# Kernel tuning notes

Measured on AMD Instinct MI355X. Metric: run time of the kernel, lower is better.

Reference implementation:

```python
import jax, jax.numpy as jnp
import numpy as np

EPS = 1e-5
DN = ('NCHW', 'OIHW', 'NCHW')


def _conv(x, w):
    return jax.lax.conv_general_dilated(x, w, (1, 1), 'SAME', dimension_numbers=DN)


def _bn(x, g, b, m, v):
    # eval-mode batchnorm over channel axis 1
    inv = jax.lax.rsqrt(v + EPS)
    return (x - m[:, None, None]) * (g * inv)[:, None, None] + b[:, None, None]


def setup_inputs() -> dict:
    key = jax.random.key(0)
    ks = jax.random.split(key, 32)
    dim, mid, B, H, W = 256, 128, 4, 128, 128
    d = {}
    d['x'] = jax.random.normal(ks[0], (B, dim, H, W), dtype=jnp.float32)

    def bn_params(i, c):
        return (jax.random.uniform(ks[i], (c,), dtype=jnp.float32) + 0.5,
                jax.random.normal(ks[i + 1], (c,), dtype=jnp.float32) * 0.1,
                jax.random.normal(ks[i + 2], (c,), dtype=jnp.float32) * 0.1,
                jax.random.uniform(ks[i + 3], (c,), dtype=jnp.float32) + 0.5)

    d['w_p1'] = jax.random.normal(ks[1], (mid, dim, 3, 3), dtype=jnp.float32) * 0.02
    d['g_p1'], d['b_p1'], d['m_p1'], d['v_p1'] = bn_params(2, mid)
    d['w_p2'] = jax.random.normal(ks[6], (mid, dim, 3, 3), dtype=jnp.float32) * 0.02
    d['g_p2'], d['b_p2'], d['m_p2'], d['v_p2'] = bn_params(7, mid)
    d['w_c1'] = jax.random.normal(ks[11], (dim, mid, 3, 3), dtype=jnp.float32) * 0.02
    d['g_c1'], d['b_c1'], d['m_c1'], d['v_c1'] = bn_params(12, dim)
    d['w_c2'] = jax.random.normal(ks[16], (dim, dim, 1, 1), dtype=jnp.float32) * 0.02
    d['g_c2'], d['b_c2'], d['m_c2'], d['v_c2'] = bn_params(17, dim)
    d['w_p3'] = jax.random.normal(ks[21], (dim, dim, 3, 3), dtype=jnp.float32) * 0.02
    d['g_p3'], d['b_p3'], d['m_p3'], d['v_p3'] = bn_params(22, dim)
    return d


def reference(x,
              w_p1, g_p1, b_p1, m_p1, v_p1,
              w_p2, g_p2, b_p2, m_p2, v_p2,
              w_c1, g_c1, b_c1, m_c1, v_c1,
              w_c2, g_c2, b_c2, m_c2, v_c2,
              w_p3, g_p3, b_p3, m_p3, v_p3):
    # conv-bn-relu branches (dim -> 128)
    p1 = jax.nn.relu(_bn(_conv(x, w_p1), g_p1, b_p1, m_p1, v_p1))
    p2 = jax.nn.relu(_bn(_conv(x, w_p2), g_p2, b_p2, m_p2, v_p2))
    # corner pooling: 'top' = reverse cummax over H (axis 2),
    #                 'left' = reverse cummax over W (axis 3)
    cp1 = jax.lax.cummax(p1, axis=2, reverse=True)
    cp2 = jax.lax.cummax(p2, axis=3, reverse=True)
    bn1 = _bn(_conv(cp1 + cp2, w_c1), g_c1, b_c1, m_c1, v_c1)
    bn2 = _bn(_conv(x, w_c2), g_c2, b_c2, m_c2, v_c2)
    r = jax.nn.relu(bn1 + bn2)
    out = jax.nn.relu(_bn(_conv(r, w_p3), g_p3, b_p3, m_p3, v_p3))
    return out
```

## Files before the change

### kernel.cpp

```cpp
#include <hip/hip_runtime.h>
#include <math.h>

#define HH 128
#define WW 128
#define HWSZ (128*128)

typedef __attribute__((ext_vector_type(8))) short short8;
typedef __attribute__((ext_vector_type(4))) float float4v;

__device__ inline short f2bf(float f) {
  unsigned x = __float_as_uint(f);
  unsigned r = (x + 0x7fffu + ((x >> 16) & 1u)) >> 16;
  return (short)r;
}
__device__ inline float bf2f(unsigned short u) {
  return __uint_as_float(((unsigned)u) << 16);
}
__device__ inline int swz(int row, int g) {
  return row * 32 + ((g ^ ((row >> 1) & 3)) << 3);
}

__global__ __launch_bounds__(256) void xcvt_kernel(const float* __restrict__ x,
                                                   short* __restrict__ xbf) {
  __shared__ short tile[32 * 264];
  const int t = threadIdx.x;
  const int h = blockIdx.x, b = blockIdx.y;
  for (int wc = 0; wc < 4; wc++) {
    const int w0 = wc * 32;
    __syncthreads();
    #pragma unroll
    for (int coi = 0; coi < 8; coi++) {
      int ci = coi * 32 + (t >> 3);
      int wq = t & 7;
      float4v f = *(const float4v*)&x[((size_t)b * 256 + ci) * HWSZ + h * WW + w0 + wq * 4];
      tile[(wq * 4 + 0) * 264 + ci] = f2bf(f.x);
      tile[(wq * 4 + 1) * 264 + ci] = f2bf(f.y);
      tile[(wq * 4 + 2) * 264 + ci] = f2bf(f.z);
      tile[(wq * 4 + 3) * 264 + ci] = f2bf(f.w);
    }
    __syncthreads();
    #pragma unroll
    for (int pass = 0; pass < 4; pass++) {
      int wl = pass * 8 + (t >> 5);
      int ci8 = (t & 31) * 8;
      short8 v = *(const short8*)&tile[wl * 264 + ci8];
      *(short8*)&xbf[(((size_t)b * HH + h) * WW + w0 + wl) * 256 + ci8] = v;
    }
  }
}

__global__ void wcvt3_kernel(const float* __restrict__ w, const float* __restrict__ g,
                             const float* __restrict__ v, short* __restrict__ out,
                             int Cin, int CoutW, int co_off) {
  int idx = blockIdx.x * blockDim.x + threadIdx.x;
  int total = CoutW * Cin * 9;
  if (idx >= total) return;
  int t  = idx % 9;
  int ci = (idx / 9) % Cin;
  int co = idx / (9 * Cin);
  float s = g[co] * rsqrtf(v[co] + 1e-5f);
  out[((size_t)t * 256 + co_off + co) * Cin + ci] = f2bf(w[idx] * s);
}

__global__ void wcvt1_kernel(const float* __restrict__ w, const float* __restrict__ g,
                             const float* __restrict__ v, short* __restrict__ out,
                             int Cin, int CoutW) {
  int idx = blockIdx.x * blockDim.x + threadIdx.x;
  if (idx >= CoutW * Cin) return;
  int co = idx / Cin;
  float s = g[co] * rsqrtf(v[co] + 1e-5f);
  out[idx] = f2bf(w[idx] * s);
}

template<int CIN_A, bool PHASE_B, int SHIFT_MODE, bool SPLIT_OUT, bool OUT_F32>
__global__ __launch_bounds__(256, 2) void conv_mfma(
    const short* __restrict__ srcA, const short* __restrict__ xB,
    const short* __restrict__ wbA, const short* __restrict__ wbB,
    const float* __restrict__ g0, const float* __restrict__ b0,
    const float* __restrict__ m0, const float* __restrict__ v0,
    const float* __restrict__ g1, const float* __restrict__ b1,
    const float* __restrict__ m1, const float* __restrict__ v1,
    void* __restrict__ out0, void* __restrict__ out1)
{
  __shared__ short A_s[130 * 32];
  __shared__ short B_s[3 * 256 * 32];

  const int tid  = threadIdx.x;
  const int wave = tid >> 6;
  const int lane = tid & 63;
  const int wm = wave & 1;
  const int wn = wave >> 1;
  const int lr = lane & 15;
  const int lk = lane >> 4;

  const int h  = blockIdx.x & 127;
  const int b  = blockIdx.x >> 7;

  constexpr int ncA = CIN_A / 32;
  const int dystart = (h == 0) ? 1 : 0;
  const int dyend   = (h == HH - 1) ? 2 : 3;
  const int chunksA = (dyend - dystart) * ncA;
  const int total   = chunksA + (PHASE_B ? 8 : 0);

  float4v acc[4][8];
  #pragma unroll
  for (int i = 0; i < 4; i++)
    #pragma unroll
    for (int j = 0; j < 8; j++) acc[i][j] = (float4v)(0.0f);

  short8 rA[3], rB[12];
  const short* aRow = nullptr;
  const short* bBase = nullptr;
  bool curIsA = true;

  auto decode = [&](int t, const short*& ar, const short*& bb, bool& isA) {
    isA = (t < chunksA);
    if (isA) {
      int dy  = dystart + t / ncA;
      int ci0 = (t % ncA) * 32;
      ar = srcA + (((size_t)b * HH + (h + dy - 1)) * WW) * CIN_A + ci0;
      bb = wbA + ((size_t)(dy * 3) * 256) * CIN_A + ci0;
    } else {
      int ci0 = (t - chunksA) * 32;
      ar = xB + (((size_t)b * HH + h) * WW) * 256 + ci0;
      bb = wbB + ci0;
    }
  };

  auto loadRegs = [&](const short* ar, const short* bb, bool isA) {
    if (isA) {
      #pragma unroll
      for (int i = 0; i < 2; i++) {
        int idx = tid + i * 256;
        int w = (idx >> 2) - 1, q = idx & 3;
        rA[i] = ((unsigned)w < (unsigned)WW)
                  ? *(const short8*)(ar + (size_t)w * CIN_A + q * 8) : (short8)(0);
      }
      if (tid < 8) {
        int idx = tid + 512;
        int w = (idx >> 2) - 1, q = idx & 3;
        rA[2] = ((unsigned)w < (unsigned)WW)
                  ? *(const short8*)(ar + (size_t)w * CIN_A + q * 8) : (short8)(0);
      }
      #pragma unroll
      for (int i = 0; i < 12; i++) {
        int idx = tid + i * 256;
        int dx = idx >> 10, rem = idx & 1023;
        int co = rem >> 2, q = rem & 3;
        rB[i] = *(const short8*)(bb + (size_t)(dx * 256 + co) * CIN_A + q * 8);
      }
    } else {
      #pragma unroll
      for (int i = 0; i < 2; i++) {
        int idx = tid + i * 256;
        int wp = idx >> 2, q = idx & 3;
        rA[i] = *(const short8*)(ar + (size_t)wp * 256 + q * 8);
      }
      #pragma unroll
      for (int i = 0; i < 4; i++) {
        int idx = tid + i * 256;
        int co = idx >> 2, q = idx & 3;
        rB[i] = *(const short8*)(bb + (size_t)co * 256 + q * 8);
      }
    }
  };

  auto storeLDS = [&](bool isA) {
    if (isA) {
      #pragma unroll
      for (int i = 0; i < 2; i++) {
        int idx = tid + i * 256;
        *(short8*)&A_s[swz(idx >> 2, idx & 3)] = rA[i];
      }
      if (tid < 8) {
        int idx = tid + 512;
        *(short8*)&A_s[swz(idx >> 2, idx & 3)] = rA[2];
      }
      #pragma unroll
      for (int i = 0; i < 12; i++) {
        int idx = tid + i * 256;
        int dx = idx >> 10, rem = idx & 1023;
        *(short8*)&B_s[swz(dx * 256 + (rem >> 2), rem & 3)] = rB[i];
      }
    } else {
      #pragma unroll
      for (int i = 0; i < 2; i++) {
        int idx = tid + i * 256;
        *(short8*)&A_s[swz(idx >> 2, idx & 3)] = rA[i];
      }
      #pragma unroll
      for (int i = 0; i < 4; i++) {
        int idx = tid + i * 256;
        *(short8*)&B_s[swz(idx >> 2, idx & 3)] = rB[i];
      }
    }
  };

  decode(0, aRow, bBase, curIsA);
  loadRegs(aRow, bBase, curIsA);

  for (int t = 0; t < total; t++) {
    bool isA = curIsA;
    __syncthreads();
    storeLDS(isA);
    __syncthreads();
    if (t + 1 < total) {
      decode(t + 1, aRow, bBase, curIsA);
      loadRegs(aRow, bBase, curIsA);
    }
    const int ndx = isA ? 3 : 1;
    for (int dx = 0; dx < ndx; dx++) {
      short8 af[4];
      #pragma unroll
      for (int mi = 0; mi < 4; mi++)
        af[mi] = *(const short8*)&A_s[swz(wm * 64 + mi * 16 + lr + dx, lk)];
      #pragma unroll
      for (int ni = 0; ni < 8; ni++) {
        short8 bfr = *(const short8*)&B_s[swz(dx * 256 + wn * 128 + ni * 16 + lr, lk)];
        #pragma unroll
        for (int mi = 0; mi < 4; mi++)
          acc[mi][ni] = __builtin_amdgcn_mfma_f32_16x16x32_bf16(af[mi], bfr, acc[mi][ni], 0, 0, 0);
      }
    }
  }

  #pragma unroll
  for (int ni = 0; ni < 8; ni++) {
    int c = wn * 128 + ni * 16 + lr;
    float sh;
    if (SHIFT_MODE == 0) {
      float s = g0[c] * rsqrtf(v0[c] + 1e-5f);
      sh = b0[c] - m0[c] * s;
    } else if (SHIFT_MODE == 1) {
      int cc = c & 127;
      const float* gg = (c < 128) ? g0 : g1;
      const float* bb = (c < 128) ? b0 : b1;
      const float* mm = (c < 128) ? m0 : m1;
      const float* vv = (c < 128) ? v0 : v1;
      float s = gg[cc] * rsqrtf(vv[cc] + 1e-5f);
      sh = bb[cc] - mm[cc] * s;
    } else {
      float s0 = g0[c] * rsqrtf(v0[c] + 1e-5f);
      float s1 = g1[c] * rsqrtf(v1[c] + 1e-5f);
      sh = (b0[c] - m0[c] * s0) + (b1[c] - m1[c] * s1);
    }
    #pragma unroll
    for (int mi = 0; mi < 4; mi++) {
      int px = wm * 64 + mi * 16 + lk * 4;
      float4v v = acc[mi][ni];
      v.x = fmaxf(v.x + sh, 0.0f);
      v.y = fmaxf(v.y + sh, 0.0f);
      v.z = fmaxf(v.z + sh, 0.0f);
      v.w = fmaxf(v.w + sh, 0.0f);
      if (OUT_F32) {
        float* ob = (float*)out0;
        *(float4v*)(ob + ((size_t)b * 256 + c) * HWSZ + (size_t)h * WW + px) = v;
      } else if (SPLIT_OUT) {
        short* ob = (short*)((c < 128) ? out0 : out1);
        size_t base = (((size_t)b * HH + h) * WW + px) * 128 + (c & 127);
        ob[base      ] = f2bf(v.x);
        ob[base + 128 ] = f2bf(v.y);
        ob[base + 256 ] = f2bf(v.z);
        ob[base + 384 ] = f2bf(v.w);
      } else {
        short* ob = (short*)out0;
        size_t base = (((size_t)b * HH + h) * WW + px) * 256 + c;
        ob[base      ] = f2bf(v.x);
        ob[base + 256 ] = f2bf(v.y);
        ob[base + 512 ] = f2bf(v.z);
        ob[base + 768 ] = f2bf(v.w);
      }
    }
  }
}

__global__ void colscan_kernel(unsigned* __restrict__ p) {
  const int t = threadIdx.x;
  const int wl = t >> 6, cp = t & 63;
  const int w = blockIdx.x * 4 + wl;
  const int b = blockIdx.y;
  float m0 = -INFINITY, m1 = -INFINITY;
  for (int h = HH - 1; h >= 0; h--) {
    size_t idx = (((size_t)b * HH + h) * WW + w) * 64 + cp;
    unsigned u = p[idx];
    float f0 = bf2f((unsigned short)(u & 0xffff));
    float f1 = bf2f((unsigned short)(u >> 16));
    m0 = fmaxf(m0, f0);
    m1 = fmaxf(m1, f1);
    p[idx] = ((unsigned)(unsigned short)f2bf(m1) << 16) | (unsigned short)f2bf(m0);
  }
}

__global__ __launch_bounds__(256) void rowscan_add_kernel(
    const short* __restrict__ p2, short* __restrict__ p1) {
  __shared__ short pl[128 * 128];
  const int tid = threadIdx.x;
  const int hb = blockIdx.x;
  const int b  = blockIdx.y;
  const size_t base = (((size_t)b * HH + hb) * WW) * 128;

  #pragma unroll
  for (int i = 0; i < 8; i++) {
    int idx = tid + i * 256;
    *(short8*)&pl[idx * 8] = *(const short8*)(p2 + base + (size_t)idx * 8);
  }
  __syncthreads();
  if (tid < 128) {
    float m = -INFINITY;
    for (int w = WW - 1; w >= 0; w--) {
      int a = w * 128 + tid;
      m = fmaxf(m, bf2f((unsigned short)pl[a]));
      pl[a] = (short)f2bf(m);
    }
  }
  __syncthreads();
  #pragma unroll
  for (int i = 0; i < 8; i++) {
    int idx = tid + i * 256;
    short8 sv = *(const short8*)&pl[idx * 8];
    short8 ov = *(const short8*)(p1 + base + (size_t)idx * 8);
    short8 rv;
    #pragma unroll
    for (int j = 0; j < 8; j++)
      rv[j] = f2bf(bf2f((unsigned short)sv[j]) + bf2f((unsigned short)ov[j]));
    *(short8*)(p1 + base + (size_t)idx * 8) = rv;
  }
}

extern "C" void kernel_launch(void* const* d_in, const int* in_sizes, int n_in,
                              void* d_out, int out_size, void* d_ws, size_t ws_size,
                              hipStream_t stream) {
  const float* x    = (const float*)d_in[0];
  const float* w_p1 = (const float*)d_in[1];
  const float* g_p1 = (const float*)d_in[2];
  const float* b_p1 = (const float*)d_in[3];
  const float* m_p1 = (const float*)d_in[4];
  const float* v_p1 = (const float*)d_in[5];
  const float* w_p2 = (const float*)d_in[6];
  const float* g_p2 = (const float*)d_in[7];
  const float* b_p2 = (const float*)d_in[8];
  const float* m_p2 = (const float*)d_in[9];
  const float* v_p2 = (const float*)d_in[10];
  const float* w_c1 = (const float*)d_in[11];
  const float* g_c1 = (const float*)d_in[12];
  const float* b_c1 = (const float*)d_in[13];
  const float* m_c1 = (const float*)d_in[14];
  const float* v_c1 = (const float*)d_in[15];
  const float* w_c2 = (const float*)d_in[16];
  const float* g_c2 = (const float*)d_in[17];
  const float* b_c2 = (const float*)d_in[18];
  const float* m_c2 = (const float*)d_in[19];
  const float* v_c2 = (const float*)d_in[20];
  const float* w_p3 = (const float*)d_in[21];
  const float* g_p3 = (const float*)d_in[22];
  const float* b_p3 = (const float*)d_in[23];
  const float* m_p3 = (const float*)d_in[24];
  const float* v_p3 = (const float*)d_in[25];

  char* ws = (char*)d_ws;
  short* p1  = (short*)(ws + 0);
  short* p2  = (short*)(ws + 16777216);
  short* r   = (short*)(ws + 33554432);
  short* xbf = (short*)(ws + 67108864);
  short* wb12 = r;
  short* wbc1 = p2;
  short* wbc2 = (short*)(ws + 16777216 + 589824);
  short* wbp3 = p1;

  xcvt_kernel<<<dim3(128, 4), 256, 0, stream>>>(x, xbf);

  wcvt3_kernel<<<(128 * 256 * 9 + 255) / 256, 256, 0, stream>>>(w_p1, g_p1, v_p1, wb12, 256, 128, 0);
  wcvt3_kernel<<<(128 * 256 * 9 + 255) / 256, 256, 0, stream>>>(w_p2, g_p2, v_p2, wb12, 256, 128, 128);

  conv_mfma<256, false, 1, true, false><<<dim3(512), 256, 0, stream>>>(
      xbf, nullptr, wb12, nullptr,
      g_p1, b_p1, m_p1, v_p1, g_p2, b_p2, m_p2, v_p2, (void*)p1, (void*)p2);

  colscan_kernel<<<dim3(32, 4), 256, 0, stream>>>((unsigned*)p1);
  rowscan_add_kernel<<<dim3(128, 4), 256, 0, stream>>>(p2, p1);

  wcvt3_kernel<<<(256 * 128 * 9 + 255) / 256, 256, 0, stream>>>(w_c1, g_c1, v_c1, wbc1, 128, 256, 0);
  wcvt1_kernel<<<(256 * 256 + 255) / 256, 256, 0, stream>>>(w_c2, g_c2, v_c2, wbc2, 256, 256);

  conv_mfma<128, true, 2, false, false><<<dim3(512), 256, 0, stream>>>(
      p1, xbf, wbc1, wbc2,
      g_c1, b_c1, m_c1, v_c1, g_c2, b_c2, m_c2, v_c2, (void*)r, nullptr);

  wcvt3_kernel<<<(256 * 256 * 9 + 255) / 256, 256, 0, stream>>>(w_p3, g_p3, v_p3, wbp3, 256, 256, 0);

  conv_mfma<256, false, 0, false, true><<<dim3(512), 256, 0, stream>>>(
      r, nullptr, wbp3, nullptr,
      g_p3, b_p3, m_p3, v_p3, nullptr, nullptr, nullptr, nullptr, d_out, nullptr);
}
```

Baseline: 425.7 us.

## Double-buffer LDS, process two output rows per 512-thread block in conv

The conv kernel now uses 512 threads per block, with each block computing two output rows so each weight chunk loaded into LDS is reused across both rows. LDS is double-buffered: the next chunk's global loads are issued before the MFMAs, and the stores to LDS are interleaved between the dx sub-steps under s_setprio. This cuts the loop to one barrier per chunk. Block IDs are remapped to spread work across XCDs, and the grid is halved to 256 blocks. The cost is doubled LDS (about 114 KB per block) and fewer blocks, which may limit occupancy and leave a 256-CU device with only one wave of blocks.

```diff
diff --git a/kernel.cpp b/kernel.cpp
--- a/kernel.cpp
+++ b/kernel.cpp
@@ -73,17 +73,17 @@
 }
 
 template<int CIN_A, bool PHASE_B, int SHIFT_MODE, bool SPLIT_OUT, bool OUT_F32>
-__global__ __launch_bounds__(256, 2) void conv_mfma(
+__global__ __launch_bounds__(512, 2) void conv_mfma(
     const short* __restrict__ srcA, const short* __restrict__ xB,
     const short* __restrict__ wbA, const short* __restrict__ wbB,
     const float* __restrict__ g0, const float* __restrict__ b0,
-    const float* __restrict__ m0, const float* __restrict__ v0,
+    const float* __restrict__ m0, const float* __restrict__ v0p,
     const float* __restrict__ g1, const float* __restrict__ b1,
-    const float* __restrict__ m1, const float* __restrict__ v1,
+    const float* __restrict__ m1, const float* __restrict__ v1p,
     void* __restrict__ out0, void* __restrict__ out1)
 {
-  __shared__ short A_s[130 * 32];
-  __shared__ short B_s[3 * 256 * 32];
+  __shared__ short A_s[2 * 8320];
+  __shared__ short B_s[2 * 24576];
 
   const int tid  = threadIdx.x;
   const int wave = tid >> 6;
@@ -93,160 +93,201 @@
   const int lr = lane & 15;
   const int lk = lane >> 4;
 
-  const int h  = blockIdx.x & 127;
-  const int b  = blockIdx.x >> 7;
+  const int raw = blockIdx.x;
+  const int id  = (raw & 7) * 32 + (raw >> 3);
+  const int h0  = (id & 63) * 2;
+  const int b   = id >> 6;
 
   constexpr int ncA = CIN_A / 32;
-  const int dystart = (h == 0) ? 1 : 0;
-  const int dyend   = (h == HH - 1) ? 2 : 3;
-  const int chunksA = (dyend - dystart) * ncA;
-  const int total   = chunksA + (PHASE_B ? 8 : 0);
-
-  float4v acc[4][8];
+  constexpr int chunksA = 3 * ncA;
+  constexpr int total = chunksA + (PHASE_B ? 8 : 0);
+
+  float4v acc[8][4];
   #pragma unroll
-  for (int i = 0; i < 4; i++)
-    #pragma unroll
-    for (int j = 0; j < 8; j++) acc[i][j] = (float4v)(0.0f);
-
-  short8 rA[3], rB[12];
-  const short* aRow = nullptr;
-  const short* bBase = nullptr;
-  bool curIsA = true;
-
-  auto decode = [&](int t, const short*& ar, const short*& bb, bool& isA) {
-    isA = (t < chunksA);
-    if (isA) {
-      int dy  = dystart + t / ncA;
-      int ci0 = (t % ncA) * 32;
-      ar = srcA + (((size_t)b * HH + (h + dy - 1)) * WW) * CIN_A + ci0;
-      bb = wbA + ((size_t)(dy * 3) * 256) * CIN_A + ci0;
+  for (int i = 0; i < 8; i++)
+    #pragma unroll
+    for (int j = 0; j < 4; j++) acc[i][j] = (float4v)(0.0f);
+
+  short8 rA[3], rB[6];
+  bool nIsA = true, av0 = false, av1 = false;
+  const short* aR = nullptr;
+  const short* bB = nullptr;
+  int r0 = 0;
+
+  auto decode = [&](int t) {
+    nIsA = (t < chunksA);
+    if (nIsA) {
+      int dy = t / ncA, ci0 = (t % ncA) * 32;
+      r0  = h0 + dy - 1;
+      av0 = (r0 >= 0);
+      av1 = (r0 + 1 <= HH - 1);
+      aR = srcA + ((size_t)b * HH) * WW * CIN_A + ci0;
+      bB = wbA + (size_t)(dy * 3) * 256 * CIN_A + ci0;
     } else {
       int ci0 = (t - chunksA) * 32;
-      ar = xB + (((size_t)b * HH + h) * WW) * 256 + ci0;
-      bb = wbB + ci0;
-    }
-  };
-
-  auto loadRegs = [&](const short* ar, const short* bb, bool isA) {
+      aR = xB + (((size_t)b * HH + h0) * WW) * 256 + ci0;
+      bB = wbB + ci0;
+    }
+  };
+
+  auto issueLoads = [&]() {
+    if (nIsA) {
+      int rr0 = av0 ? r0 : 0;
+      int rr1 = av1 ? r0 + 1 : 0;
+      { int g = tid; int w = (g >> 2) - 1, q = g & 3;
+        rA[0] = (av0 && (unsigned)w < (unsigned)WW)
+            ? *(const short8*)(aR + ((size_t)rr0 * WW + w) * CIN_A + q * 8) : (short8)(0); }
+      { int g = tid + 512; int pl = (g >= 520) ? 1 : 0; int gg = g - pl * 520;
+        int w = (gg >> 2) - 1, q = gg & 3;
+        bool vv = pl ? av1 : av0; int rr = pl ? rr1 : rr0;
+        rA[1] = (vv && (unsigned)w < (unsigned)WW)
+            ? *(const short8*)(aR + ((size_t)rr * WW + w) * CIN_A + q * 8) : (short8)(0); }
+      if (tid < 16) { int gg = tid + 504; int w = (gg >> 2) - 1, q = gg & 3;
+        rA[2] = (av1 && (unsigned)w < (unsigned)WW)
+            ? *(const short8*)(aR + ((size_t)rr1 * WW + w) * CIN_A + q * 8) : (short8)(0); }
+      #pragma unroll
+      for (int i = 0; i < 6; i++) {
+        int idx = tid + i * 512;
+        int dx = idx >> 10, rem = idx & 1023, co = rem >> 2, q = rem & 3;
+        rB[i] = *(const short8*)(bB + (size_t)(dx * 256 + co) * CIN_A + q * 8);
+      }
+    } else {
+      #pragma unroll
+      for (int i = 0; i < 2; i++) {
+        int idx = tid + i * 512; int pl = idx >> 9, rem = idx & 511, w = rem >> 2, q = rem & 3;
+        rA[i] = *(const short8*)(aR + ((size_t)pl * WW + w) * 256 + q * 8);
+      }
+      #pragma unroll
+      for (int i = 0; i < 2; i++) {
+        int idx = tid + i * 512; int co = idx >> 2, q = idx & 3;
+        rB[i] = *(const short8*)(bB + (size_t)co * 256 + q * 8);
+      }
+    }
+  };
+
+  int cur = 1;
+
+  auto storeP0 = [&]() {
+    short* Ab = A_s + (cur ^ 1) * 8320;
+    short* Bb = B_s + (cur ^ 1) * 24576;
+    if (nIsA) {
+      { int g = tid; *(short8*)&Ab[swz(g >> 2, g & 3)] = rA[0]; }
+      { int g = tid + 512; int pl = (g >= 520) ? 1 : 0; int gg = g - pl * 520;
+        *(short8*)&Ab[pl * 4160 + swz(gg >> 2, gg & 3)] = rA[1]; }
+      if (tid < 16) { int gg = tid + 504;
+        *(short8*)&Ab[4160 + swz(gg >> 2, gg & 3)] = rA[2]; }
+      #pragma unroll
+      for (int i = 0; i < 2; i++) {
+        int idx = tid + i * 512; int dx = idx >> 10, rem = idx & 1023;
+        *(short8*)&Bb[swz(dx * 256 + (rem >> 2), rem & 3)] = rB[i];
+      }
+    } else {
+      #pragma unroll
+      for (int i = 0; i < 2; i++) {
+        int idx = tid + i * 512; int pl = idx >> 9, rem = idx & 511;
+        *(short8*)&Ab[pl * 4160 + swz(rem >> 2, rem & 3)] = rA[i];
+      }
+      #pragma unroll
+      for (int i = 0; i < 2; i++) {
+        int idx = tid + i * 512;
+        *(short8*)&Bb[swz(idx >> 2, idx & 3)] = rB[i];
+      }
+    }
+  };
+  auto storeP1 = [&]() {
+    if (!nIsA) return;
+    short* Bb = B_s + (cur ^ 1) * 24576;
+    #pragma unroll
+    for (int i = 2; i < 4; i++) {
+      int idx = tid + i * 512; int dx = idx >> 10, rem = idx & 1023;
+      *(short8*)&Bb[swz(dx * 256 + (rem >> 2), rem & 3)] = rB[i];
+    }
+  };
+  auto storeP2 = [&]() {
+    if (!nIsA) return;
+    short* Bb = B_s + (cur ^ 1) * 24576;
+    #pragma unroll
+    for (int i = 4; i < 6; i++) {
+      int idx = tid + i * 512; int dx = idx >> 10, rem = idx & 1023;
+      *(short8*)&Bb[swz(dx * 256 + (rem >> 2), rem & 3)] = rB[i];
+    }
+  };
+
+  auto mfma_dx = [&](int dx) {
+    const short* Ab = A_s + cur * 8320 + wm * 4160;
+    const short* Bb = B_s + cur * 24576;
+    short8 bfv[4];
+    #pragma unroll
+    for (int ni = 0; ni < 4; ni++)
+      bfv[ni] = *(const short8*)&Bb[swz(dx * 256 + wn * 64 + ni * 16 + lr, lk)];
+    #pragma unroll
+    for (int mi = 0; mi < 8; mi++) {
+      short8 afv = *(const short8*)&Ab[swz(mi * 16 + lr + dx, lk)];
+      #pragma unroll
+      for (int ni = 0; ni < 4; ni++)
+        acc[mi][ni] = __builtin_amdgcn_mfma_f32_16x16x32_bf16(afv, bfv[ni], acc[mi][ni], 0, 0, 0);
+    }
+  };
+
+  decode(0);
+  issueLoads();
+  storeP0(); storeP1(); storeP2();
+  asm volatile("s_waitcnt lgkmcnt(0)" ::: "memory");
+  __builtin_amdgcn_s_barrier();
+  __builtin_amdgcn_sched_barrier(0);
+  cur = 0;
+
+  #pragma unroll 1
+  for (int t = 0; t < total; t++) {
+    const bool isA = (t < chunksA);
+    const bool hnext = (t + 1 < total);
+    if (hnext) { decode(t + 1); issueLoads(); }
+
+    __builtin_amdgcn_s_setprio(1);
+    mfma_dx(0);
+    __builtin_amdgcn_s_setprio(0);
+    if (hnext) storeP0();
     if (isA) {
-      #pragma unroll
-      for (int i = 0; i < 2; i++) {
-        int idx = tid + i * 256;
-        int w = (idx >> 2) - 1, q = idx & 3;
-        rA[i] = ((unsigned)w < (unsigned)WW)
-                  ? *(const short8*)(ar + (size_t)w * CIN_A + q * 8) : (short8)(0);
-      }
-      if (tid < 8) {
-        int idx = tid + 512;
-        int w = (idx >> 2) - 1, q = idx & 3;
-        rA[2] = ((unsigned)w < (unsigned)WW)
-                  ? *(const short8*)(ar + (size_t)w * CIN_A + q * 8) : (short8)(0);
-      }
-      #pragma unroll
-      for (int i = 0; i < 12; i++) {
-        int idx = tid + i * 256;
-        int dx = idx >> 10, rem = idx & 1023;
-        int co = rem >> 2, q = rem & 3;
-        rB[i] = *(const short8*)(bb + (size_t)(dx * 256 + co) * CIN_A + q * 8);
-      }
-    } else {
-      #pragma unroll
-      for (int i = 0; i < 2; i++) {
-        int idx = tid + i * 256;
-        int wp = idx >> 2, q = idx & 3;
-        rA[i] = *(const short8*)(ar + (size_t)wp * 256 + q * 8);
-      }
-      #pragma unroll
-      for (int i = 0; i < 4; i++) {
-        int idx = tid + i * 256;
-        int co = idx >> 2, q = idx & 3;
-        rB[i] = *(const short8*)(bb + (size_t)co * 256 + q * 8);
-      }
-    }
-  };
-
-  auto storeLDS = [&](bool isA) {
-    if (isA) {
-      #pragma unroll
-      for (int i = 0; i < 2; i++) {
-        int idx = tid + i * 256;
-        *(short8*)&A_s[swz(idx >> 2, idx & 3)] = rA[i];
-      }
-      if (tid < 8) {
-        int idx = tid + 512;
-        *(short8*)&A_s[swz(idx >> 2, idx & 3)] = rA[2];
-      }
-      #pragma unroll
-      for (int i = 0; i < 12; i++) {
-        int idx = tid + i * 256;
-        int dx = idx >> 10, rem = idx & 1023;
-        *(short8*)&B_s[swz(dx * 256 + (rem >> 2), rem & 3)] = rB[i];
-      }
-    } else {
-      #pragma unroll
-      for (int i = 0; i < 2; i++) {
-        int idx = tid + i * 256;
-        *(short8*)&A_s[swz(idx >> 2, idx & 3)] = rA[i];
-      }
-      #pragma unroll
-      for (int i = 0; i < 4; i++) {
-        int idx = tid + i * 256;
-        *(short8*)&B_s[swz(idx >> 2, idx & 3)] = rB[i];
-      }
-    }
-  };
-
-  decode(0, aRow, bBase, curIsA);
-  loadRegs(aRow, bBase, curIsA);
-
-  for (int t = 0; t < total; t++) {
-    bool isA = curIsA;
-    __syncthreads();
-    storeLDS(isA);
-    __syncthreads();
-    if (t + 1 < total) {
-      decode(t + 1, aRow, bBase, curIsA);
-      loadRegs(aRow, bBase, curIsA);
-    }
-    const int ndx = isA ? 3 : 1;
-    for (int dx = 0; dx < ndx; dx++) {
-      short8 af[4];
-      #pragma unroll
-      for (int mi = 0; mi < 4; mi++)
-        af[mi] = *(const short8*)&A_s[swz(wm * 64 + mi * 16 + lr + dx, lk)];
-      #pragma unroll
-      for (int ni = 0; ni < 8; ni++) {
-        short8 bfr = *(const short8*)&B_s[swz(dx * 256 + wn * 128 + ni * 16 + lr, lk)];
-        #pragma unroll
-        for (int mi = 0; mi < 4; mi++)
-          acc[mi][ni] = __builtin_amdgcn_mfma_f32_16x16x32_bf16(af[mi], bfr, acc[mi][ni], 0, 0, 0);
-      }
-    }
-  }
-
+      __builtin_amdgcn_s_setprio(1);
+      mfma_dx(1);
+      __builtin_amdgcn_s_setprio(0);
+      if (hnext) storeP1();
+      __builtin_amdgcn_s_setprio(1);
+      mfma_dx(2);
+      __builtin_amdgcn_s_setprio(0);
+      if (hnext) storeP2();
+    } else if (hnext) { storeP1(); storeP2(); }
+
+    asm volatile("s_waitcnt lgkmcnt(0)" ::: "memory");
+    __builtin_amdgcn_s_barrier();
+    __builtin_amdgcn_sched_barrier(0);
+    cur ^= 1;
+  }
+
+  const int h2 = h0 + wm;
   #pragma unroll
-  for (int ni = 0; ni < 8; ni++) {
-    int c = wn * 128 + ni * 16 + lr;
+  for (int ni = 0; ni < 4; ni++) {
+    int c = wn * 64 + ni * 16 + lr;
     float sh;
     if (SHIFT_MODE == 0) {
-      float s = g0[c] * rsqrtf(v0[c] + 1e-5f);
+      float s = g0[c] * rsqrtf(v0p[c] + 1e-5f);
       sh = b0[c] - m0[c] * s;
     } else if (SHIFT_MODE == 1) {
       int cc = c & 127;
       const float* gg = (c < 128) ? g0 : g1;
       const float* bb = (c < 128) ? b0 : b1;
       const float* mm = (c < 128) ? m0 : m1;
-      const float* vv = (c < 128) ? v0 : v1;
+      const float* vv = (c < 128) ? v0p : v1p;
       float s = gg[cc] * rsqrtf(vv[cc] + 1e-5f);
       sh = bb[cc] - mm[cc] * s;
     } else {
-      float s0 = g0[c] * rsqrtf(v0[c] + 1e-5f);
-      float s1 = g1[c] * rsqrtf(v1[c] + 1e-5f);
+      float s0 = g0[c] * rsqrtf(v0p[c] + 1e-5f);
+      float s1 = g1[c] * rsqrtf(v1p[c] + 1e-5f);
       sh = (b0[c] - m0[c] * s0) + (b1[c] - m1[c] * s1);
     }
     #pragma unroll
-    for (int mi = 0; mi < 4; mi++) {
-      int px = wm * 64 + mi * 16 + lk * 4;
+    for (int mi = 0; mi < 8; mi++) {
+      int w = mi * 16 + lk * 4;
       float4v v = acc[mi][ni];
       v.x = fmaxf(v.x + sh, 0.0f);
       v.y = fmaxf(v.y + sh, 0.0f);
@@ -254,17 +295,17 @@
       v.w = fmaxf(v.w + sh, 0.0f);
       if (OUT_F32) {
         float* ob = (float*)out0;
-        *(float4v*)(ob + ((size_t)b * 256 + c) * HWSZ + (size_t)h * WW + px) = v;
+        *(float4v*)(ob + ((size_t)b * 256 + c) * HWSZ + (size_t)h2 * WW + w) = v;
       } else if (SPLIT_OUT) {
         short* ob = (short*)((c < 128) ? out0 : out1);
-        size_t base = (((size_t)b * HH + h) * WW + px) * 128 + (c & 127);
+        size_t base = (((size_t)b * HH + h2) * WW + w) * 128 + (c & 127);
         ob[base      ] = f2bf(v.x);
         ob[base + 128 ] = f2bf(v.y);
         ob[base + 256 ] = f2bf(v.z);
         ob[base + 384 ] = f2bf(v.w);
       } else {
         short* ob = (short*)out0;
-        size_t base = (((size_t)b * HH + h) * WW + px) * 256 + c;
+        size_t base = (((size_t)b * HH + h2) * WW + w) * 256 + c;
         ob[base      ] = f2bf(v.x);
         ob[base + 256 ] = f2bf(v.y);
         ob[base + 512 ] = f2bf(v.z);
@@ -372,7 +413,7 @@
   wcvt3_kernel<<<(128 * 256 * 9 + 255) / 256, 256, 0, stream>>>(w_p1, g_p1, v_p1, wb12, 256, 128, 0);
   wcvt3_kernel<<<(128 * 256 * 9 + 255) / 256, 256, 0, stream>>>(w_p2, g_p2, v_p2, wb12, 256, 128, 128);
 
-  conv_mfma<256, false, 1, true, false><<<dim3(512), 256, 0, stream>>>(
+  conv_mfma<256, false, 1, true, false><<<dim3(256), 512, 0, stream>>>(
       xbf, nullptr, wb12, nullptr,
       g_p1, b_p1, m_p1, v_p1, g_p2, b_p2, m_p2, v_p2, (void*)p1, (void*)p2);
 
@@ -382,13 +423,13 @@
   wcvt3_kernel<<<(256 * 128 * 9 + 255) / 256, 256, 0, stream>>>(w_c1, g_c1, v_c1, wbc1, 128, 256, 0);
   wcvt1_kernel<<<(256 * 256 + 255) / 256, 256, 0, stream>>>(w_c2, g_c2, v_c2, wbc2, 256, 256);
 
-  conv_mfma<128, true, 2, false, false><<<dim3(512), 256, 0, stream>>>(
+  conv_mfma<128, true, 2, false, false><<<dim3(256), 512, 0, stream>>>(
       p1, xbf, wbc1, wbc2,
       g_c1, b_c1, m_c1, v_c1, g_c2, b_c2, m_c2, v_c2, (void*)r, nullptr);
 
   wcvt3_kernel<<<(256 * 256 * 9 + 255) / 256, 256, 0, stream>>>(w_p3, g_p3, v_p3, wbp3, 256, 256, 0);
 
-  conv_mfma<256, false, 0, false, true><<<dim3(512), 256, 0, stream>>>(
+  conv_mfma<256, false, 0, false, true><<<dim3(256), 512, 0, stream>>>(
       r, nullptr, wbp3, nullptr,
       g_p3, b_p3, m_p3, v_p3, nullptr, nullptr, nullptr, nullptr, d_out, nullptr);
 }
```

After: 722.2 us. +69.7%, slower.

## Double-buffer LDS and interleave prefetch with MFMA in conv mainloop

Applied to the files above, without the earlier changes.

Converts the conv mainloop from a single LDS buffer with two barriers per chunk to a double-buffered LDS scheme. The next chunk's register data is stored into the alternate buffer between the per-dx MFMA groups, while global loads for the chunk after that are issued, leaving one barrier per iteration. Splitting the weight load and store into two halves spreads the memory traffic across the compute phases. This doubles LDS use to about 112 KB per block, so launch bounds drop to one block per SM and occupancy falls.

```diff
diff --git a/kernel.cpp b/kernel.cpp
--- a/kernel.cpp
+++ b/kernel.cpp
@@ -73,7 +73,7 @@
 }
 
 template<int CIN_A, bool PHASE_B, int SHIFT_MODE, bool SPLIT_OUT, bool OUT_F32>
-__global__ __launch_bounds__(256, 2) void conv_mfma(
+__global__ __launch_bounds__(256, 1) void conv_mfma(
     const short* __restrict__ srcA, const short* __restrict__ xB,
     const short* __restrict__ wbA, const short* __restrict__ wbB,
     const float* __restrict__ g0, const float* __restrict__ b0,
@@ -82,8 +82,8 @@
     const float* __restrict__ m1, const float* __restrict__ v1,
     void* __restrict__ out0, void* __restrict__ out1)
 {
-  __shared__ short A_s[130 * 32];
-  __shared__ short B_s[3 * 256 * 32];
+  __shared__ short A_s[2][130 * 32];
+  __shared__ short B_s[2][3 * 256 * 32];
 
   const int tid  = threadIdx.x;
   const int wave = tid >> 6;
@@ -109,12 +109,9 @@
     for (int j = 0; j < 8; j++) acc[i][j] = (float4v)(0.0f);
 
   short8 rA[3], rB[12];
-  const short* aRow = nullptr;
-  const short* bBase = nullptr;
-  bool curIsA = true;
-
-  auto decode = [&](int t, const short*& ar, const short*& bb, bool& isA) {
-    isA = (t < chunksA);
+
+  auto decode = [&](int t, const short*& ar, const short*& bb) -> bool {
+    bool isA = (t < chunksA);
     if (isA) {
       int dy  = dystart + t / ncA;
       int ci0 = (t % ncA) * 32;
@@ -125,9 +122,10 @@
       ar = xB + (((size_t)b * HH + h) * WW) * 256 + ci0;
       bb = wbB + ci0;
     }
-  };
-
-  auto loadRegs = [&](const short* ar, const short* bb, bool isA) {
+    return isA;
+  };
+
+  auto loadA = [&](const short* ar, bool isA) {
     if (isA) {
       #pragma unroll
       for (int i = 0; i < 2; i++) {
@@ -142,8 +140,20 @@
         rA[2] = ((unsigned)w < (unsigned)WW)
                   ? *(const short8*)(ar + (size_t)w * CIN_A + q * 8) : (short8)(0);
       }
-      #pragma unroll
-      for (int i = 0; i < 12; i++) {
+    } else {
+      #pragma unroll
+      for (int i = 0; i < 2; i++) {
+        int idx = tid + i * 256;
+        int wp = idx >> 2, q = idx & 3;
+        rA[i] = *(const short8*)(ar + (size_t)wp * 256 + q * 8);
+      }
+    }
+  };
+
+  auto loadB1 = [&](const short* bb, bool isA) {
+    if (isA) {
+      #pragma unroll
+      for (int i = 0; i < 6; i++) {
         int idx = tid + i * 256;
         int dx = idx >> 10, rem = idx & 1023;
         int co = rem >> 2, q = rem & 3;
@@ -151,12 +161,6 @@
       }
     } else {
       #pragma unroll
-      for (int i = 0; i < 2; i++) {
-        int idx = tid + i * 256;
-        int wp = idx >> 2, q = idx & 3;
-        rA[i] = *(const short8*)(ar + (size_t)wp * 256 + q * 8);
-      }
-      #pragma unroll
       for (int i = 0; i < 4; i++) {
         int idx = tid + i * 256;
         int co = idx >> 2, q = idx & 3;
@@ -165,63 +169,125 @@
     }
   };
 
-  auto storeLDS = [&](bool isA) {
+  auto loadB2 = [&](const short* bb, bool isA) {
+    if (isA) {
+      #pragma unroll
+      for (int i = 6; i < 12; i++) {
+        int idx = tid + i * 256;
+        int dx = idx >> 10, rem = idx & 1023;
+        int co = rem >> 2, q = rem & 3;
+        rB[i] = *(const short8*)(bb + (size_t)(dx * 256 + co) * CIN_A + q * 8);
+      }
+    }
+  };
+
+  auto storeA = [&](int buf, bool isA) {
+    short* As = A_s[buf];
     if (isA) {
       #pragma unroll
       for (int i = 0; i < 2; i++) {
         int idx = tid + i * 256;
-        *(short8*)&A_s[swz(idx >> 2, idx & 3)] = rA[i];
+        *(short8*)&As[swz(idx >> 2, idx & 3)] = rA[i];
       }
       if (tid < 8) {
         int idx = tid + 512;
-        *(short8*)&A_s[swz(idx >> 2, idx & 3)] = rA[2];
-      }
-      #pragma unroll
-      for (int i = 0; i < 12; i++) {
+        *(short8*)&As[swz(idx >> 2, idx & 3)] = rA[2];
+      }
+    } else {
+      #pragma unroll
+      for (int i = 0; i < 2; i++) {
+        int idx = tid + i * 256;
+        *(short8*)&As[swz(idx >> 2, idx & 3)] = rA[i];
+      }
+    }
+  };
+
+  auto storeB1 = [&](int buf, bool isA) {
+    short* Bs = B_s[buf];
+    if (isA) {
+      #pragma unroll
+      for (int i = 0; i < 6; i++) {
         int idx = tid + i * 256;
         int dx = idx >> 10, rem = idx & 1023;
-        *(short8*)&B_s[swz(dx * 256 + (rem >> 2), rem & 3)] = rB[i];
-      }
-    } else {
-      #pragma unroll
-      for (int i = 0; i < 2; i++) {
-        int idx = tid + i * 256;
-        *(short8*)&A_s[swz(idx >> 2, idx & 3)] = rA[i];
-      }
+        *(short8*)&Bs[swz(dx * 256 + (rem >> 2), rem & 3)] = rB[i];
+      }
+    } else {
       #pragma unroll
       for (int i = 0; i < 4; i++) {
         int idx = tid + i * 256;
-        *(short8*)&B_s[swz(idx >> 2, idx & 3)] = rB[i];
-      }
-    }
-  };
-
-  decode(0, aRow, bBase, curIsA);
-  loadRegs(aRow, bBase, curIsA);
-
+        *(short8*)&Bs[swz(idx >> 2, idx & 3)] = rB[i];
+      }
+    }
+  };
+
+  auto storeB2 = [&](int buf, bool isA) {
+    short* Bs = B_s[buf];
+    if (isA) {
+      #pragma unroll
+      for (int i = 6; i < 12; i++) {
+        int idx = tid + i * 256;
+        int dx = idx >> 10, rem = idx & 1023;
+        *(short8*)&Bs[swz(dx * 256 + (rem >> 2), rem & 3)] = rB[i];
+      }
+    }
+  };
+
+  auto mfma_dx = [&](int buf, int dx) {
+    short8 af[4];
+    #pragma unroll
+    for (int mi = 0; mi < 4; mi++)
+      af[mi] = *(const short8*)&A_s[buf][swz(wm * 64 + mi * 16 + lr + dx, lk)];
+    #pragma unroll
+    for (int ni = 0; ni < 8; ni++) {
+      short8 bfr = *(const short8*)&B_s[buf][swz(dx * 256 + wn * 128 + ni * 16 + lr, lk)];
+      #pragma unroll
+      for (int mi = 0; mi < 4; mi++)
+        acc[mi][ni] = __builtin_amdgcn_mfma_f32_16x16x32_bf16(af[mi], bfr, acc[mi][ni], 0, 0, 0);
+    }
+  };
+
+  {
+    const short* ar; const short* bb;
+    bool ia0 = decode(0, ar, bb);
+    loadA(ar, ia0); loadB1(bb, ia0); loadB2(bb, ia0);
+    storeA(0, ia0); storeB1(0, ia0); storeB2(0, ia0);
+    if (total > 1) {
+      const short* ar1; const short* bb1;
+      bool ia1 = decode(1, ar1, bb1);
+      loadA(ar1, ia1); loadB1(bb1, ia1); loadB2(bb1, ia1);
+    }
+    asm volatile("s_waitcnt lgkmcnt(0)" ::: "memory");
+    __builtin_amdgcn_s_barrier();
+    __builtin_amdgcn_sched_barrier(0);
+  }
+
+  int cur = 0;
+  #pragma unroll 1
   for (int t = 0; t < total; t++) {
-    bool isA = curIsA;
-    __syncthreads();
-    storeLDS(isA);
-    __syncthreads();
-    if (t + 1 < total) {
-      decode(t + 1, aRow, bBase, curIsA);
-      loadRegs(aRow, bBase, curIsA);
-    }
-    const int ndx = isA ? 3 : 1;
-    for (int dx = 0; dx < ndx; dx++) {
-      short8 af[4];
-      #pragma unroll
-      for (int mi = 0; mi < 4; mi++)
-        af[mi] = *(const short8*)&A_s[swz(wm * 64 + mi * 16 + lr + dx, lk)];
-      #pragma unroll
-      for (int ni = 0; ni < 8; ni++) {
-        short8 bfr = *(const short8*)&B_s[swz(dx * 256 + wn * 128 + ni * 16 + lr, lk)];
-        #pragma unroll
-        for (int mi = 0; mi < 4; mi++)
-          acc[mi][ni] = __builtin_amdgcn_mfma_f32_16x16x32_bf16(af[mi], bfr, acc[mi][ni], 0, 0, 0);
-      }
-    }
+    const bool isA = (t < chunksA);
+    const bool h1  = (t + 1 < total);
+    const bool sA  = (t + 1 < chunksA);
+    const bool h2  = (t + 2 < total);
+
+    const short* ar2 = nullptr; const short* bb2 = nullptr; bool ia2 = false;
+    if (h2) ia2 = decode(t + 2, ar2, bb2);
+
+    mfma_dx(cur, 0);
+    if (h1) storeA(cur ^ 1, sA);
+    if (h2) loadA(ar2, ia2);
+
+    if (isA) mfma_dx(cur, 1);
+    if (h1) storeB1(cur ^ 1, sA);
+    if (h2) loadB1(bb2, ia2);
+
+    if (isA) mfma_dx(cur, 2);
+    if (h1) storeB2(cur ^ 1, sA);
+    if (h2) loadB2(bb2, ia2);
+
+    asm volatile("s_waitcnt lgkmcnt(0)" ::: "memory");
+    __builtin_amdgcn_s_barrier();
+    __builtin_amdgcn_sched_barrier(0);
+    cur ^= 1;
   }
 
   #pragma unroll
```

Result: slower. 520.9 us (+22.4%).

## Parallelize corner-pool scans with wavefront shuffle prefix-max in LDS

Applied to the files above, without the earlier changes.

Both the column (top) and row (left) reverse cummax kernels now stage a 128x128 slice into padded float LDS and run a wavefront-wide suffix-max scan using shuffles over two 64-element halves. Previously the column scan ran 128 sequential strided global loads per thread with only 128 blocks, and the row scan used only 128 of 256 threads doing a serial 128-step loop. The change targets these latency-bound serial scans. In exchange it adds 66 KB of LDS per block, which limits occupancy, and adds extra shuffle work.

```diff
diff --git a/kernel.cpp b/kernel.cpp
--- a/kernel.cpp
+++ b/kernel.cpp
@@ -274,26 +274,57 @@
   }
 }
 
-__global__ void colscan_kernel(unsigned* __restrict__ p) {
-  const int t = threadIdx.x;
-  const int wl = t >> 6, cp = t & 63;
-  const int w = blockIdx.x * 4 + wl;
+__global__ __launch_bounds__(256) void colscan_kernel(short* __restrict__ p) {
+  __shared__ float xf[128 * 129];
+  const int tid = threadIdx.x;
+  const int w = blockIdx.x;
   const int b = blockIdx.y;
-  float m0 = -INFINITY, m1 = -INFINITY;
-  for (int h = HH - 1; h >= 0; h--) {
-    size_t idx = (((size_t)b * HH + h) * WW + w) * 64 + cp;
-    unsigned u = p[idx];
-    float f0 = bf2f((unsigned short)(u & 0xffff));
-    float f1 = bf2f((unsigned short)(u >> 16));
-    m0 = fmaxf(m0, f0);
-    m1 = fmaxf(m1, f1);
-    p[idx] = ((unsigned)(unsigned short)f2bf(m1) << 16) | (unsigned short)f2bf(m0);
+  const size_t base = (size_t)b * HH * WW * 128 + (size_t)w * 128;
+
+  #pragma unroll
+  for (int i = 0; i < 8; i++) {
+    int idx = tid + i * 256;
+    int h = idx >> 4, g = idx & 15;
+    short8 v = *(const short8*)(p + base + (size_t)h * (WW * 128) + g * 8);
+    #pragma unroll
+    for (int j = 0; j < 8; j++) xf[h * 129 + g * 8 + j] = bf2f((unsigned short)v[j]);
+  }
+  __syncthreads();
+
+  const int lane = tid & 63, wv = tid >> 6;
+  for (int rep = 0; rep < 32; rep++) {
+    int c = rep * 4 + wv;
+    float lo = xf[lane * 129 + c];
+    float hi = xf[(lane + 64) * 129 + c];
+    #pragma unroll
+    for (int off = 1; off < 64; off <<= 1) {
+      int src = lane + off; if (src > 63) src = 63;
+      float ul = __shfl(lo, src);
+      float uh = __shfl(hi, src);
+      lo = fmaxf(lo, ul);
+      hi = fmaxf(hi, uh);
+    }
+    float ht = __shfl(hi, 0);
+    lo = fmaxf(lo, ht);
+    xf[lane * 129 + c] = lo;
+    xf[(lane + 64) * 129 + c] = hi;
+  }
+  __syncthreads();
+
+  #pragma unroll
+  for (int i = 0; i < 8; i++) {
+    int idx = tid + i * 256;
+    int h = idx >> 4, g = idx & 15;
+    short8 v;
+    #pragma unroll
+    for (int j = 0; j < 8; j++) v[j] = f2bf(xf[h * 129 + g * 8 + j]);
+    *(short8*)(p + base + (size_t)h * (WW * 128) + g * 8) = v;
   }
 }
 
 __global__ __launch_bounds__(256) void rowscan_add_kernel(
     const short* __restrict__ p2, short* __restrict__ p1) {
-  __shared__ short pl[128 * 128];
+  __shared__ float pf[128 * 129];
   const int tid = threadIdx.x;
   const int hb = blockIdx.x;
   const int b  = blockIdx.y;
@@ -302,27 +333,42 @@
   #pragma unroll
   for (int i = 0; i < 8; i++) {
     int idx = tid + i * 256;
-    *(short8*)&pl[idx * 8] = *(const short8*)(p2 + base + (size_t)idx * 8);
+    int w = idx >> 4, g = idx & 15;
+    short8 v = *(const short8*)(p2 + base + (size_t)idx * 8);
+    #pragma unroll
+    for (int j = 0; j < 8; j++) pf[w * 129 + g * 8 + j] = bf2f((unsigned short)v[j]);
   }
   __syncthreads();
-  if (tid < 128) {
-    float m = -INFINITY;
-    for (int w = WW - 1; w >= 0; w--) {
-      int a = w * 128 + tid;
-      m = fmaxf(m, bf2f((unsigned short)pl[a]));
-      pl[a] = (short)f2bf(m);
-    }
+
+  const int lane = tid & 63, wv = tid >> 6;
+  for (int rep = 0; rep < 32; rep++) {
+    int c = rep * 4 + wv;
+    float lo = pf[lane * 129 + c];
+    float hi = pf[(lane + 64) * 129 + c];
+    #pragma unroll
+    for (int off = 1; off < 64; off <<= 1) {
+      int src = lane + off; if (src > 63) src = 63;
+      float ul = __shfl(lo, src);
+      float uh = __shfl(hi, src);
+      lo = fmaxf(lo, ul);
+      hi = fmaxf(hi, uh);
+    }
+    float ht = __shfl(hi, 0);
+    lo = fmaxf(lo, ht);
+    pf[lane * 129 + c] = lo;
+    pf[(lane + 64) * 129 + c] = hi;
   }
   __syncthreads();
+
   #pragma unroll
   for (int i = 0; i < 8; i++) {
     int idx = tid + i * 256;
-    short8 sv = *(const short8*)&pl[idx * 8];
+    int w = idx >> 4, g = idx & 15;
     short8 ov = *(const short8*)(p1 + base + (size_t)idx * 8);
     short8 rv;
     #pragma unroll
     for (int j = 0; j < 8; j++)
-      rv[j] = f2bf(bf2f((unsigned short)sv[j]) + bf2f((unsigned short)ov[j]));
+      rv[j] = f2bf(pf[w * 129 + g * 8 + j] + bf2f((unsigned short)ov[j]));
     *(short8*)(p1 + base + (size_t)idx * 8) = rv;
   }
 }
@@ -376,7 +422,7 @@
       xbf, nullptr, wb12, nullptr,
       g_p1, b_p1, m_p1, v_p1, g_p2, b_p2, m_p2, v_p2, (void*)p1, (void*)p2);
 
-  colscan_kernel<<<dim3(32, 4), 256, 0, stream>>>((unsigned*)p1);
+  colscan_kernel<<<dim3(128, 4), 256, 0, stream>>>(p1);
   rowscan_add_kernel<<<dim3(128, 4), 256, 0, stream>>>(p2, p1);
 
   wcvt3_kernel<<<(256 * 128 * 9 + 255) / 256, 256, 0, stream>>>(w_c1, g_c1, v_c1, wbc1, 128, 256, 0);
```

Result: slower. 436.7 us (+2.6%).
